# Kernel optimization log

Hardware: AMD Instinct MI355X
Metric: run time of the kernel (lower is better)

## Reference

```python
import jax, jax.numpy as jnp
import numpy as np

B, N, F, H = 1, 778, 128, 8
D = F // H        # per-head dim (d_q = d_v = 16)
D2 = 2 * D        # attn-mlp hidden channels per head (grouped conv: 2*f_dim / H)
EPS = 1e-6


def setup_inputs() -> dict:
    key = jax.random.key(0)
    ks = jax.random.split(key, 16)
    s = 0.02
    def lin(k, i, o):
        return jax.random.normal(k, (i, o), jnp.float32) * s
    f32 = jnp.float32
    return {
        "Lf": jax.random.normal(ks[0], (B, N, F), f32),
        "Rf": jax.random.normal(ks[1], (B, N, F), f32),
        "left_pos": jax.random.normal(ks[2], (B, N, F), f32),
        "right_pos": jax.random.normal(ks[3], (B, N, F), f32),
        # pos_mlp: Linear(F,2F) -> ReLU -> Linear(2F,F)
        "pos_W1": lin(ks[4], F, 2 * F), "pos_b1": jnp.zeros((2 * F,), f32),
        "pos_W2": lin(ks[5], 2 * F, F), "pos_b2": jnp.zeros((F,), f32),
        # q/k/v projections (F -> H*D = F)
        "Wq": lin(ks[6], F, F), "bq": jnp.zeros((F,), f32),
        "Wv": lin(ks[7], F, F), "bv": jnp.zeros((F,), f32),
        "Wk": lin(ks[8], F, F), "bk": jnp.zeros((F,), f32),
        # attn_mlp: grouped 1x1 convs == per-head linear maps D->D2->D
        "conv1_w": jax.random.normal(ks[9], (H, D2, D), f32) * s, "conv1_b": jnp.zeros((H, D2), f32),
        "conv2_w": jax.random.normal(ks[10], (H, D, D2), f32) * s, "conv2_b": jnp.zeros((H, D), f32),
        # ffL = MLP_res_block: LayerNorm + Linear(F,2F)->ReLU->Linear(2F,F) + residual
        "ln_g": jnp.ones((F,), f32), "ln_b": jnp.zeros((F,), f32),
        "ff_W1": lin(ks[11], F, 2 * F), "ff_b1": jnp.zeros((2 * F,), f32),
        "ff_W2": lin(ks[12], 2 * F, F), "ff_b2": jnp.zeros((F,), f32),
    }


def reference(Lf, Rf, left_pos, right_pos,
              pos_W1, pos_b1, pos_W2, pos_b2,
              Wq, bq, Wv, bv, Wk, bk,
              conv1_w, conv1_b, conv2_w, conv2_b,
              ln_g, ln_b, ff_W1, ff_b1, ff_W2, ff_b2):
    b, n, f = Lf.shape
    # pairwise relative positions -> per-pair embedding via pos MLP
    rel_pos = left_pos[:, :, None, :] - right_pos[:, None, :, :]          # (b,i,j,F)
    rel = jax.nn.relu(rel_pos @ pos_W1 + pos_b1) @ pos_W2 + pos_b2        # (b,i,j,F)
    rel = rel.reshape(b, n, n, H, D)                                       # (b,i,j,h,d)
    Lq = (Lf @ Wq + bq).reshape(b, n, H, D)
    Lv = (Lf @ Wv + bv).reshape(b, n, H, D)
    Rk = (Rf @ Wk + bk).reshape(b, n, H, D)
    # subtraction-based pairwise scores + rel-pos embedding
    x = Lq[:, :, None] - Rk[:, None, :] + rel                              # (b,i,j,h,d)
    # grouped 1x1 convs == independent per-head linears over channel d
    hid = jax.nn.relu(jnp.einsum('bijhd,hod->bijho', x, conv1_w) + conv1_b)
    sim = jnp.einsum('bijho,hdo->bijhd', hid, conv2_w) + conv2_b           # (b,i,j,h,d)
    # torch softmax(dim=-2) on (b, h*d, i, j) -> over i
    attn = jax.nn.softmax(sim, axis=1)
    # NOTE: v = repeat(Lv, 'b h j d -> b h i j d') broadcasts Lv over i (indexed by j)
    v = Lv[:, None] + rel                                                  # (b,i,j,h,d)
    agg = jnp.einsum('bijhd,bijhd->bihd', attn, v).reshape(b, n, f)        # sum over j
    y = Lf + agg  # dropout is identity in eval
    # MLP_res_block: x + fc2(relu(fc1(LN(x))))
    mu = jnp.mean(y, axis=-1, keepdims=True)
    var = jnp.var(y, axis=-1, keepdims=True)
    yn = (y - mu) / jnp.sqrt(var + EPS) * ln_g + ln_b
    return y + (jax.nn.relu(yn @ ff_W1 + ff_b1) @ ff_W2 + ff_b2)
```

## Files before the change

### kernel.cpp

```cpp
#include <hip/hip_runtime.h>
#include <hip/hip_bf16.h>

#define NROW 778
#define NPAD 784
#define FDIM 128
#define KHID 256

typedef unsigned short u16;
typedef __attribute__((ext_vector_type(4))) unsigned int u32x4;
typedef __attribute__((ext_vector_type(4))) float f32x4;

__device__ __forceinline__ u16 f2bfu(float x) {
  return __builtin_bit_cast(u16, __float2bfloat16(x));
}

__device__ __forceinline__ void mfma_bf16(f32x4& d, const u32x4& a, const u32x4& b) {
  asm("v_mfma_f32_16x16x32_bf16 %0, %1, %2, %0" : "+v"(d) : "v"(a), "v"(b));
}

#define WS_A    0u
#define WS_C    802816u
#define WS_XI   1605632u
#define WS_XJ   2007040u
#define WS_VJ   2408448u
#define WS_S    2809856u
#define WS_INV  3211264u
#define WS_AGG  3612672u
#define WS_W2B  4014080u
#define WS_C1B  4079616u
#define WS_C2B  4096000u

#define SM_A    0
#define SM_CF   16384
#define SM_W2B  32768
#define SM_HID  0
#define SM_XJ   65536
#define SM_SP   73728
#define SM_INVS 73728
#define SM_VJ   81920
#define SM_C1B  98304
#define SM_C2B  114688
#define SM_X    122880
#define SM_CB1  155648
#define SM_CB2  156672
#define SM_TOTAL 157184

__global__ void kzero(float* S, float* agg) {
  int idx = blockIdx.x * blockDim.x + threadIdx.x;
  if (idx < NPAD * FDIM) { S[idx] = 0.f; agg[idx] = 0.f; }
}

__global__ void kinv(const float* __restrict__ S, float* __restrict__ invS) {
  int idx = blockIdx.x * blockDim.x + threadIdx.x;
  if (idx >= NPAD * FDIM) return;
  int j = idx >> 7;
  invS[idx] = (j < NROW) ? 1.f / S[idx] : 0.f;
}

__global__ void kprep_rows(const float* __restrict__ Lf, const float* __restrict__ Rf,
                           const float* __restrict__ lp, const float* __restrict__ rp,
                           const float* __restrict__ W1, const float* __restrict__ b1,
                           const float* __restrict__ b2,
                           const float* __restrict__ Wq, const float* __restrict__ bq,
                           const float* __restrict__ Wv, const float* __restrict__ bv,
                           const float* __restrict__ Wk, const float* __restrict__ bk,
                           float* __restrict__ a, float* __restrict__ c,
                           float* __restrict__ xi, float* __restrict__ xj,
                           float* __restrict__ vj) {
  __shared__ float sl[128], sr[128], slp[128], srp[128];
  const int row = blockIdx.x, t = threadIdx.x;
  if (t < 128) {
    sl[t] = Lf[row * 128 + t]; sr[t] = Rf[row * 128 + t];
    slp[t] = lp[row * 128 + t]; srp[t] = rp[row * 128 + t];
  }
  __syncthreads();
  float aa = 0.f, cc = 0.f;
  for (int k = 0; k < 128; ++k) {
    float w = W1[k * 256 + t];
    aa += slp[k] * w; cc += srp[k] * w;
  }
  a[row * 256 + t] = aa;
  c[row * 256 + t] = b1[t] - cc;
  if (t < 128) {
    float q = 0.f, kk = 0.f, vv = 0.f;
    for (int k = 0; k < 128; ++k) {
      float l = sl[k], r = sr[k];
      q  += l * Wq[k * 128 + t];
      vv += l * Wv[k * 128 + t];
      kk += r * Wk[k * 128 + t];
    }
    xi[row * 128 + t] = q + bq[t] + b2[t];
    xj[row * 128 + t] = -(kk + bk[t]);
    vj[row * 128 + t] = vv + bv[t] + b2[t];
  }
}

__global__ void kprep_frags(const float* __restrict__ W2, const float* __restrict__ c1w,
                            const float* __restrict__ c2w,
                            u16* __restrict__ w2B, u16* __restrict__ c1B,
                            u16* __restrict__ c2B) {
  const int idx0 = blockIdx.x * blockDim.x + threadIdx.x;
  const int nthr = gridDim.x * blockDim.x;
  for (int idx = idx0; idx < 32768; idx += nthr) {
    int e = idx & 7, ln = (idx >> 3) & 63, n = (idx >> 9) & 7, ks = idx >> 12;
    int k = ks * 32 + ((ln >> 4) << 3) + e;
    int col = n * 16 + (ln & 15);
    w2B[idx] = f2bfu(W2[k * FDIM + col]);
  }
  for (int idx = idx0; idx < 8192; idx += nthr) {
    int e = idx & 7, ln = (idx >> 3) & 63, b = (idx >> 9) & 3, hp = idx >> 11;
    int k = ((ln >> 4) << 3) + e;
    int col = ln & 15;
    int hb = hp * 2 + (b >> 1);
    float v = ((k >> 4) == (b >> 1)) ? c1w[(hb * 32 + (b & 1) * 16 + col) * 16 + (k & 15)] : 0.f;
    c1B[idx] = f2bfu(v);
  }
  for (int idx = idx0; idx < 4096; idx += nthr) {
    int e = idx & 7, ln = (idx >> 3) & 63, h = idx >> 9;
    int o = ((ln >> 4) << 3) + e;
    int d = ln & 15;
    c2B[idx] = f2bfu(c2w[(h * 16 + d) * 32 + o]);
  }
}

template <int PASS>
__global__ __launch_bounds__(512, 2) void kpass(
    const float* __restrict__ ga, const float* __restrict__ gc,
    const float* __restrict__ gxi, const float* __restrict__ gxj,
    const float* __restrict__ gvj, const u16* __restrict__ gw2B,
    const u16* __restrict__ gc1B, const u16* __restrict__ gc2B,
    const float* __restrict__ gcb1, const float* __restrict__ gcb2,
    float* __restrict__ S, const float* __restrict__ invS, float* __restrict__ agg) {
  __shared__ __align__(16) char sm[SM_TOTAL];
  float* sA   = (float*)(sm + SM_A);
  float* sCf  = (float*)(sm + SM_CF);
  u16*   sW2B = (u16*)(sm + SM_W2B);
  u16*   sHid = (u16*)(sm + SM_HID);
  float* sXj  = (float*)(sm + SM_XJ);
  float* sSp  = (float*)(sm + SM_SP);
  float* sInvS= (float*)(sm + SM_INVS);
  float* sVj  = (float*)(sm + SM_VJ);
  u16*   sC1B = (u16*)(sm + SM_C1B);
  u16*   sC2B = (u16*)(sm + SM_C2B);
  u16*   sX   = (u16*)(sm + SM_X);
  float* sCB1 = (float*)(sm + SM_CB1);
  float* sCB2 = (float*)(sm + SM_CB2);

  const int tid = threadIdx.x;
  const int lane = tid & 63;
  const int w = tid >> 6;
  const int jj = lane & 15, kg = lane >> 4;
  const int i0 = blockIdx.x * 16, j0 = blockIdx.y * 16;

  for (int idx = tid; idx < 4096; idx += 512) {
    int row = idx >> 8;
    int ir = i0 + row; if (ir > NROW - 1) ir = NROW - 1;
    sA[idx] = ga[ir * KHID + (idx & 255)];
  }
  for (int idx = tid; idx < 4096; idx += 512) {
    int ks = idx >> 9, ln = (idx >> 3) & 63, e = idx & 7;
    int jr = j0 + (ln & 15); if (jr > NROW - 1) jr = NROW - 1;
    int k = ks * 32 + ((ln >> 4) << 3) + e;
    sCf[idx] = gc[jr * KHID + k];
  }
  {
    const u32x4* g = (const u32x4*)gw2B; u32x4* s = (u32x4*)sW2B;
    for (int idx = tid; idx < 4096; idx += 512) s[idx] = g[idx];
    const u32x4* g1 = (const u32x4*)gc1B; u32x4* s1 = (u32x4*)sC1B;
    for (int idx = tid; idx < 1024; idx += 512) s1[idx] = g1[idx];
    const u32x4* g2 = (const u32x4*)gc2B; u32x4* s2 = (u32x4*)sC2B;
    s2[tid] = g2[tid];
    if (tid < 256) sCB1[tid] = gcb1[tid];
    else if (tid < 384) sCB2[tid - 256] = gcb2[tid - 256];
  }
  __syncthreads();

  f32x4 acc[2][8];
#pragma unroll
  for (int mt = 0; mt < 2; ++mt)
#pragma unroll
    for (int n = 0; n < 8; ++n) acc[mt][n] = f32x4{0.f, 0.f, 0.f, 0.f};

#pragma unroll
  for (int ks = 0; ks < 8; ++ks) {
    const float4 c0 = *(const float4*)&sCf[(ks * 64 + lane) * 8];
    const float4 c1 = *(const float4*)&sCf[(ks * 64 + lane) * 8 + 4];
    const int ko = ks * 32 + kg * 8;
    u32x4 A[2];
#pragma unroll
    for (int mt = 0; mt < 2; ++mt) {
      const float4 a0 = *(const float4*)&sA[(2 * w + mt) * KHID + ko];
      const float4 a1 = *(const float4*)&sA[(2 * w + mt) * KHID + ko + 4];
      float h0 = fmaxf(a0.x + c0.x, 0.f), h1 = fmaxf(a0.y + c0.y, 0.f);
      float h2 = fmaxf(a0.z + c0.z, 0.f), h3 = fmaxf(a0.w + c0.w, 0.f);
      float h4 = fmaxf(a1.x + c1.x, 0.f), h5 = fmaxf(a1.y + c1.y, 0.f);
      float h6 = fmaxf(a1.z + c1.z, 0.f), h7 = fmaxf(a1.w + c1.w, 0.f);
      A[mt] = u32x4{(unsigned)f2bfu(h0) | ((unsigned)f2bfu(h1) << 16),
                    (unsigned)f2bfu(h2) | ((unsigned)f2bfu(h3) << 16),
                    (unsigned)f2bfu(h4) | ((unsigned)f2bfu(h5) << 16),
                    (unsigned)f2bfu(h6) | ((unsigned)f2bfu(h7) << 16)};
    }
#pragma unroll
    for (int n = 0; n < 8; ++n) {
      u32x4 B = ((const u32x4*)sW2B)[(ks * 8 + n) * 64 + lane];
      mfma_bf16(acc[0][n], A[0], B);
      mfma_bf16(acc[1][n], A[1], B);
    }
  }
  __syncthreads();

  if (PASS == 0) {
    for (int idx = tid; idx < 2048; idx += 512) sSp[idx] = 0.f;
  } else {
    for (int idx = tid; idx < 2048; idx += 512) {
      int row = idx >> 7, ch = idx & 127;
      int jr = j0 + row;
      sInvS[idx] = invS[jr * FDIM + ch];
      int jc = jr > NROW - 1 ? NROW - 1 : jr;
      sVj[idx] = gvj[jc * FDIM + ch];
    }
  }
  for (int idx = tid; idx < 2048; idx += 512) {
    int row = idx >> 7, ch = idx & 127;
    int jr = j0 + row; if (jr > NROW - 1) jr = NROW - 1;
    sXj[idx] = gxj[jr * FDIM + ch];
  }
  __syncthreads();

  u16* myX = sX + w * 2048;
  u16* myH = sHid + w * 4096;
#pragma unroll
  for (int mt = 0; mt < 2; ++mt) {
    const int i = i0 + 2 * w + mt;
    const int ic = i > NROW - 1 ? NROW - 1 : i;
#pragma unroll
    for (int n = 0; n < 8; ++n) {
      const int ch = n * 16 + jj;
      const float xiv = gxi[ic * FDIM + ch];
#pragma unroll
      for (int r = 0; r < 4; ++r) {
        const int prow = kg * 4 + r;
        float xv = acc[mt][n][r] + xiv + sXj[prow * FDIM + ch];
        int idxX = ((ch >> 5) * 512) + (prow + 16 * ((ch >> 3) & 3)) * 8 + (ch & 7);
        myX[idxX] = f2bfu(xv);
      }
    }
#pragma unroll
    for (int hp = 0; hp < 4; ++hp) {
      u32x4 Ax = ((const u32x4*)myX)[hp * 64 + lane];
#pragma unroll
      for (int b = 0; b < 4; ++b) {
        u32x4 Bw = ((const u32x4*)sC1B)[(hp * 4 + b) * 64 + lane];
        f32x4 hacc = f32x4{0.f, 0.f, 0.f, 0.f};
        mfma_bf16(hacc, Ax, Bw);
        const int och = (hp * 2 + (b >> 1)) * 32 + (b & 1) * 16 + jj;
        const float bias = sCB1[och];
#pragma unroll
        for (int r = 0; r < 4; ++r) {
          const int prow = kg * 4 + r;
          float hv = fmaxf(hacc[r] + bias, 0.f);
          int idxH = ((och >> 5) * 512) + (prow + 16 * ((och >> 3) & 3)) * 8 + (och & 7);
          myH[idxH] = f2bfu(hv);
        }
      }
    }
#pragma unroll
    for (int h = 0; h < 8; ++h) {
      u32x4 Ah = ((const u32x4*)myH)[h * 64 + lane];
      u32x4 Bw = ((const u32x4*)sC2B)[h * 64 + lane];
      f32x4 sacc = f32x4{0.f, 0.f, 0.f, 0.f};
      mfma_bf16(sacc, Ah, Bw);
      const float bias = sCB2[h * 16 + jj];
      if (PASS == 0) {
        if (i < NROW) {
#pragma unroll
          for (int r = 0; r < 4; ++r) {
            float e = __expf(sacc[r] + bias);
            atomicAdd(&sSp[(kg * 4 + r) * FDIM + h * 16 + jj], e);
          }
        }
      } else {
        float sum = 0.f;
#pragma unroll
        for (int r = 0; r < 4; ++r) {
          const int prow = kg * 4 + r;
          float e = __expf(sacc[r] + bias);
          float iv = sInvS[prow * FDIM + h * 16 + jj];
          float vv = acc[mt][h][r] + sVj[prow * FDIM + h * 16 + jj];
          sum += e * iv * vv;
        }
        sum += __shfl_xor(sum, 16);
        sum += __shfl_xor(sum, 32);
        if (lane < 16) atomicAdd(&agg[i * FDIM + h * 16 + lane], sum);
      }
    }
  }
  if (PASS == 0) {
    __syncthreads();
    for (int idx = tid; idx < 2048; idx += 512) {
      int row = idx >> 7;
      atomicAdd(&S[(j0 + row) * FDIM + (idx & 127)], sSp[idx]);
    }
  }
}

__global__ void kfinal(const float* __restrict__ Lf, const float* __restrict__ agg,
                       const float* __restrict__ g, const float* __restrict__ b,
                       const float* __restrict__ W1, const float* __restrict__ b1,
                       const float* __restrict__ W2, const float* __restrict__ b2,
                       float* __restrict__ out) {
  __shared__ float sY[128], sYn[128], sH[256], sStat[2];
  const int row = blockIdx.x, t = threadIdx.x;
  if (t < 128) sY[t] = Lf[row * 128 + t] + agg[row * 128 + t];
  __syncthreads();
  if (t < 64) {
    float y0 = sY[t], y1 = sY[t + 64];
    float s = y0 + y1, s2 = y0 * y0 + y1 * y1;
#pragma unroll
    for (int off = 32; off; off >>= 1) {
      s += __shfl_down(s, off);
      s2 += __shfl_down(s2, off);
    }
    if (t == 0) {
      float mu = s * (1.f / 128.f);
      float var = s2 * (1.f / 128.f) - mu * mu;
      sStat[0] = mu;
      sStat[1] = rsqrtf(var + 1e-6f);
    }
  }
  __syncthreads();
  if (t < 128) sYn[t] = (sY[t] - sStat[0]) * sStat[1] * g[t] + b[t];
  __syncthreads();
  float ha = b1[t];
  for (int k = 0; k < 128; ++k) ha += sYn[k] * W1[k * 256 + t];
  sH[t] = fmaxf(ha, 0.f);
  __syncthreads();
  if (t < 128) {
    float oa = b2[t];
    for (int k = 0; k < 256; ++k) oa += sH[k] * W2[k * 128 + t];
    out[row * 128 + t] = sY[t] + oa;
  }
}

extern "C" void kernel_launch(void* const* d_in, const int* in_sizes, int n_in,
                              void* d_out, int out_size, void* d_ws, size_t ws_size,
                              hipStream_t stream) {
  const float* Lf  = (const float*)d_in[0];
  const float* Rf  = (const float*)d_in[1];
  const float* lp  = (const float*)d_in[2];
  const float* rp  = (const float*)d_in[3];
  const float* pW1 = (const float*)d_in[4];
  const float* pb1 = (const float*)d_in[5];
  const float* pW2 = (const float*)d_in[6];
  const float* pb2 = (const float*)d_in[7];
  const float* Wq  = (const float*)d_in[8];
  const float* bq  = (const float*)d_in[9];
  const float* Wv  = (const float*)d_in[10];
  const float* bv  = (const float*)d_in[11];
  const float* Wk  = (const float*)d_in[12];
  const float* bk  = (const float*)d_in[13];
  const float* c1w = (const float*)d_in[14];
  const float* c1b = (const float*)d_in[15];
  const float* c2w = (const float*)d_in[16];
  const float* c2b = (const float*)d_in[17];
  const float* lng = (const float*)d_in[18];
  const float* lnb = (const float*)d_in[19];
  const float* fW1 = (const float*)d_in[20];
  const float* fb1 = (const float*)d_in[21];
  const float* fW2 = (const float*)d_in[22];
  const float* fb2 = (const float*)d_in[23];
  float* out = (float*)d_out;
  char* ws = (char*)d_ws;

  float* a    = (float*)(ws + WS_A);
  float* c    = (float*)(ws + WS_C);
  float* xi   = (float*)(ws + WS_XI);
  float* xj   = (float*)(ws + WS_XJ);
  float* vj   = (float*)(ws + WS_VJ);
  float* S    = (float*)(ws + WS_S);
  float* invS = (float*)(ws + WS_INV);
  float* agg  = (float*)(ws + WS_AGG);
  u16* w2B = (u16*)(ws + WS_W2B);
  u16* c1B = (u16*)(ws + WS_C1B);
  u16* c2B = (u16*)(ws + WS_C2B);

  kzero<<<dim3((NPAD * FDIM + 511) / 512), dim3(512), 0, stream>>>(S, agg);
  kprep_rows<<<dim3(NROW), dim3(256), 0, stream>>>(Lf, Rf, lp, rp, pW1, pb1, pb2,
                                                   Wq, bq, Wv, bv, Wk, bk,
                                                   a, c, xi, xj, vj);
  kprep_frags<<<dim3(16), dim3(512), 0, stream>>>(pW2, c1w, c2w, w2B, c1B, c2B);

  kpass<0><<<dim3(49, 49), dim3(512), 0, stream>>>(a, c, xi, xj, vj, w2B, c1B, c2B,
                                                   c1b, c2b, S, invS, agg);
  kinv<<<dim3((NPAD * FDIM + 511) / 512), dim3(512), 0, stream>>>(S, invS);
  kpass<1><<<dim3(49, 49), dim3(512), 0, stream>>>(a, c, xi, xj, vj, w2B, c1B, c2B,
                                                   c1b, c2b, S, invS, agg);
  kfinal<<<dim3(NROW), dim3(256), 0, stream>>>(Lf, agg, lng, lnb, fW1, fb1, fW2, fb2, out);
}
```

Measured before the change: 756.1 us.

## Make pass kernels persistent over tile strips with register accumulation

Shrinks each pass grid from 49x49 to 49x5 blocks. Each block keeps one tile fixed (j in pass 0, i in pass 1) and loops over a strided set of the other-axis tiles, so the fixed operand is loaded once per block. Softmax denominators and aggregation partials now accumulate in registers across iterations, which removes most shared and global atomics. Weight fragments and biases are read straight from global memory instead of being staged in LDS, trading global/L2 traffic for less staging work. The cost is only 245 blocks per pass, which risks underfilling the GPU and adds serial work per block.

```diff
diff --git a/kernel.cpp b/kernel.cpp
--- a/kernel.cpp
+++ b/kernel.cpp
@@ -13,8 +13,7 @@
 __device__ __forceinline__ u16 f2bfu(float x) {
   return __builtin_bit_cast(u16, __float2bfloat16(x));
 }
-
-__device__ __forceinline__ void mfma_bf16(f32x4& d, const u32x4& a, const u32x4& b) {
+__device__ __forceinline__ void mfma32(f32x4& d, const u32x4& a, const u32x4& b) {
   asm("v_mfma_f32_16x16x32_bf16 %0, %1, %2, %0" : "+v"(d) : "v"(a), "v"(b));
 }
 
@@ -29,21 +28,6 @@
 #define WS_W2B  4014080u
 #define WS_C1B  4079616u
 #define WS_C2B  4096000u
-
-#define SM_A    0
-#define SM_CF   16384
-#define SM_W2B  32768
-#define SM_HID  0
-#define SM_XJ   65536
-#define SM_SP   73728
-#define SM_INVS 73728
-#define SM_VJ   81920
-#define SM_C1B  98304
-#define SM_C2B  114688
-#define SM_X    122880
-#define SM_CB1  155648
-#define SM_CB2  156672
-#define SM_TOTAL 157184
 
 __global__ void kzero(float* S, float* agg) {
   int idx = blockIdx.x * blockDim.x + threadIdx.x;
@@ -131,175 +115,217 @@
     const u16* __restrict__ gc1B, const u16* __restrict__ gc2B,
     const float* __restrict__ gcb1, const float* __restrict__ gcb2,
     float* __restrict__ S, const float* __restrict__ invS, float* __restrict__ agg) {
-  __shared__ __align__(16) char sm[SM_TOTAL];
-  float* sA   = (float*)(sm + SM_A);
-  float* sCf  = (float*)(sm + SM_CF);
-  u16*   sW2B = (u16*)(sm + SM_W2B);
-  u16*   sHid = (u16*)(sm + SM_HID);
-  float* sXj  = (float*)(sm + SM_XJ);
-  float* sSp  = (float*)(sm + SM_SP);
-  float* sInvS= (float*)(sm + SM_INVS);
-  float* sVj  = (float*)(sm + SM_VJ);
-  u16*   sC1B = (u16*)(sm + SM_C1B);
-  u16*   sC2B = (u16*)(sm + SM_C2B);
-  u16*   sX   = (u16*)(sm + SM_X);
-  float* sCB1 = (float*)(sm + SM_CB1);
-  float* sCB2 = (float*)(sm + SM_CB2);
+  __shared__ __align__(16) char sm[155648];
+  float* sA  = (float*)(sm + 0);
+  float* sCf = (float*)(sm + 16384);
+  float* sXj = (float*)(sm + 131072);
+  float* sIv = (float*)(sm + 139264);
+  float* sVj = (float*)(sm + 147456);
 
   const int tid = threadIdx.x;
   const int lane = tid & 63;
   const int w = tid >> 6;
   const int jj = lane & 15, kg = lane >> 4;
-  const int i0 = blockIdx.x * 16, j0 = blockIdx.y * 16;
-
-  for (int idx = tid; idx < 4096; idx += 512) {
-    int row = idx >> 8;
-    int ir = i0 + row; if (ir > NROW - 1) ir = NROW - 1;
-    sA[idx] = ga[ir * KHID + (idx & 255)];
-  }
-  for (int idx = tid; idx < 4096; idx += 512) {
-    int ks = idx >> 9, ln = (idx >> 3) & 63, e = idx & 7;
-    int jr = j0 + (ln & 15); if (jr > NROW - 1) jr = NROW - 1;
-    int k = ks * 32 + ((ln >> 4) << 3) + e;
-    sCf[idx] = gc[jr * KHID + k];
-  }
-  {
-    const u32x4* g = (const u32x4*)gw2B; u32x4* s = (u32x4*)sW2B;
-    for (int idx = tid; idx < 4096; idx += 512) s[idx] = g[idx];
-    const u32x4* g1 = (const u32x4*)gc1B; u32x4* s1 = (u32x4*)sC1B;
-    for (int idx = tid; idx < 1024; idx += 512) s1[idx] = g1[idx];
-    const u32x4* g2 = (const u32x4*)gc2B; u32x4* s2 = (u32x4*)sC2B;
-    s2[tid] = g2[tid];
-    if (tid < 256) sCB1[tid] = gcb1[tid];
-    else if (tid < 384) sCB2[tid - 256] = gcb2[tid - 256];
-  }
-  __syncthreads();
-
-  f32x4 acc[2][8];
-#pragma unroll
-  for (int mt = 0; mt < 2; ++mt)
-#pragma unroll
-    for (int n = 0; n < 8; ++n) acc[mt][n] = f32x4{0.f, 0.f, 0.f, 0.f};
-
-#pragma unroll
-  for (int ks = 0; ks < 8; ++ks) {
-    const float4 c0 = *(const float4*)&sCf[(ks * 64 + lane) * 8];
-    const float4 c1 = *(const float4*)&sCf[(ks * 64 + lane) * 8 + 4];
-    const int ko = ks * 32 + kg * 8;
-    u32x4 A[2];
-#pragma unroll
-    for (int mt = 0; mt < 2; ++mt) {
-      const float4 a0 = *(const float4*)&sA[(2 * w + mt) * KHID + ko];
-      const float4 a1 = *(const float4*)&sA[(2 * w + mt) * KHID + ko + 4];
-      float h0 = fmaxf(a0.x + c0.x, 0.f), h1 = fmaxf(a0.y + c0.y, 0.f);
-      float h2 = fmaxf(a0.z + c0.z, 0.f), h3 = fmaxf(a0.w + c0.w, 0.f);
-      float h4 = fmaxf(a1.x + c1.x, 0.f), h5 = fmaxf(a1.y + c1.y, 0.f);
-      float h6 = fmaxf(a1.z + c1.z, 0.f), h7 = fmaxf(a1.w + c1.w, 0.f);
-      A[mt] = u32x4{(unsigned)f2bfu(h0) | ((unsigned)f2bfu(h1) << 16),
-                    (unsigned)f2bfu(h2) | ((unsigned)f2bfu(h3) << 16),
-                    (unsigned)f2bfu(h4) | ((unsigned)f2bfu(h5) << 16),
-                    (unsigned)f2bfu(h6) | ((unsigned)f2bfu(h7) << 16)};
-    }
-#pragma unroll
-    for (int n = 0; n < 8; ++n) {
-      u32x4 B = ((const u32x4*)sW2B)[(ks * 8 + n) * 64 + lane];
-      mfma_bf16(acc[0][n], A[0], B);
-      mfma_bf16(acc[1][n], A[1], B);
-    }
-  }
-  __syncthreads();
+  const int fix0 = blockIdx.x * 16;
+  const int s = blockIdx.y;
+
+  u16* myX = (u16*)(sm + 32768 + w * 12288);
+  u16* myH = (u16*)(sm + 32768 + w * 12288 + 4096);
+  const u32x4* w2v = (const u32x4*)gw2B;
+  const u32x4* c1v = (const u32x4*)gc1B;
+  const u32x4* c2v = (const u32x4*)gc2B;
 
   if (PASS == 0) {
-    for (int idx = tid; idx < 2048; idx += 512) sSp[idx] = 0.f;
-  } else {
+    const int j0 = fix0;
+    for (int idx = tid; idx < 4096; idx += 512) {
+      int ks = idx >> 9, ln = (idx >> 3) & 63, e = idx & 7;
+      int jr = j0 + (ln & 15); if (jr > NROW - 1) jr = NROW - 1;
+      int k = ks * 32 + ((ln >> 4) << 3) + e;
+      sCf[idx] = gc[jr * KHID + k];
+    }
     for (int idx = tid; idx < 2048; idx += 512) {
       int row = idx >> 7, ch = idx & 127;
-      int jr = j0 + row;
-      sInvS[idx] = invS[jr * FDIM + ch];
-      int jc = jr > NROW - 1 ? NROW - 1 : jr;
-      sVj[idx] = gvj[jc * FDIM + ch];
-    }
-  }
-  for (int idx = tid; idx < 2048; idx += 512) {
-    int row = idx >> 7, ch = idx & 127;
-    int jr = j0 + row; if (jr > NROW - 1) jr = NROW - 1;
-    sXj[idx] = gxj[jr * FDIM + ch];
-  }
-  __syncthreads();
-
-  u16* myX = sX + w * 2048;
-  u16* myH = sHid + w * 4096;
-#pragma unroll
-  for (int mt = 0; mt < 2; ++mt) {
-    const int i = i0 + 2 * w + mt;
-    const int ic = i > NROW - 1 ? NROW - 1 : i;
-#pragma unroll
-    for (int n = 0; n < 8; ++n) {
-      const int ch = n * 16 + jj;
-      const float xiv = gxi[ic * FDIM + ch];
-#pragma unroll
-      for (int r = 0; r < 4; ++r) {
-        const int prow = kg * 4 + r;
-        float xv = acc[mt][n][r] + xiv + sXj[prow * FDIM + ch];
-        int idxX = ((ch >> 5) * 512) + (prow + 16 * ((ch >> 3) & 3)) * 8 + (ch & 7);
-        myX[idxX] = f2bfu(xv);
-      }
-    }
-#pragma unroll
-    for (int hp = 0; hp < 4; ++hp) {
-      u32x4 Ax = ((const u32x4*)myX)[hp * 64 + lane];
-#pragma unroll
-      for (int b = 0; b < 4; ++b) {
-        u32x4 Bw = ((const u32x4*)sC1B)[(hp * 4 + b) * 64 + lane];
-        f32x4 hacc = f32x4{0.f, 0.f, 0.f, 0.f};
-        mfma_bf16(hacc, Ax, Bw);
-        const int och = (hp * 2 + (b >> 1)) * 32 + (b & 1) * 16 + jj;
-        const float bias = sCB1[och];
+      int jr = j0 + row; if (jr > NROW - 1) jr = NROW - 1;
+      sXj[idx] = gxj[jr * FDIM + ch];
+    }
+  } else {
+    const int i0 = fix0;
+    for (int idx = tid; idx < 4096; idx += 512) {
+      int row = idx >> 8;
+      int ir = i0 + row; if (ir > NROW - 1) ir = NROW - 1;
+      sA[idx] = ga[ir * KHID + (idx & 255)];
+    }
+  }
+
+  float ssum[8][4];
+  f32x4 asum[2][2];
+  float aacc[2][8];
+#pragma unroll
+  for (int h = 0; h < 8; ++h)
+#pragma unroll
+    for (int r = 0; r < 4; ++r) ssum[h][r] = 0.f;
+#pragma unroll
+  for (int mt = 0; mt < 2; ++mt)
+#pragma unroll
+    for (int h = 0; h < 8; ++h) aacc[mt][h] = 0.f;
+  (void)asum;
+
+  for (int t = s; t < 49; t += 5) {
+    const int i0 = (PASS == 0) ? t * 16 : fix0;
+    const int j0 = (PASS == 0) ? fix0 : t * 16;
+    if (PASS == 0) {
+      for (int idx = tid; idx < 4096; idx += 512) {
+        int row = idx >> 8;
+        int ir = i0 + row; if (ir > NROW - 1) ir = NROW - 1;
+        sA[idx] = ga[ir * KHID + (idx & 255)];
+      }
+    } else {
+      for (int idx = tid; idx < 4096; idx += 512) {
+        int ks = idx >> 9, ln = (idx >> 3) & 63, e = idx & 7;
+        int jr = j0 + (ln & 15); if (jr > NROW - 1) jr = NROW - 1;
+        int k = ks * 32 + ((ln >> 4) << 3) + e;
+        sCf[idx] = gc[jr * KHID + k];
+      }
+      for (int idx = tid; idx < 2048; idx += 512) {
+        int row = idx >> 7, ch = idx & 127;
+        int jr = j0 + row; if (jr > NROW - 1) jr = NROW - 1;
+        sXj[idx] = gxj[jr * FDIM + ch];
+      }
+      for (int idx = tid; idx < 2048; idx += 512) {
+        int row = idx >> 7, ch = idx & 127;
+        int jr = j0 + row;
+        sIv[idx] = invS[jr * FDIM + ch];
+        int jc = jr > NROW - 1 ? NROW - 1 : jr;
+        sVj[idx] = gvj[jc * FDIM + ch];
+      }
+    }
+    __syncthreads();
+
+    f32x4 acc[2][8];
+#pragma unroll
+    for (int mt = 0; mt < 2; ++mt)
+#pragma unroll
+      for (int n = 0; n < 8; ++n) acc[mt][n] = f32x4{0.f, 0.f, 0.f, 0.f};
+
+#pragma unroll
+    for (int ks = 0; ks < 8; ++ks) {
+      const float4 c0 = *(const float4*)&sCf[(ks * 64 + lane) * 8];
+      const float4 c1 = *(const float4*)&sCf[(ks * 64 + lane) * 8 + 4];
+      const int ko = ks * 32 + kg * 8;
+      u32x4 A[2];
+#pragma unroll
+      for (int mt = 0; mt < 2; ++mt) {
+        const float4 a0 = *(const float4*)&sA[(2 * w + mt) * KHID + ko];
+        const float4 a1 = *(const float4*)&sA[(2 * w + mt) * KHID + ko + 4];
+        float h0 = fmaxf(a0.x + c0.x, 0.f), h1 = fmaxf(a0.y + c0.y, 0.f);
+        float h2 = fmaxf(a0.z + c0.z, 0.f), h3 = fmaxf(a0.w + c0.w, 0.f);
+        float h4 = fmaxf(a1.x + c1.x, 0.f), h5 = fmaxf(a1.y + c1.y, 0.f);
+        float h6 = fmaxf(a1.z + c1.z, 0.f), h7 = fmaxf(a1.w + c1.w, 0.f);
+        A[mt] = u32x4{(unsigned)f2bfu(h0) | ((unsigned)f2bfu(h1) << 16),
+                      (unsigned)f2bfu(h2) | ((unsigned)f2bfu(h3) << 16),
+                      (unsigned)f2bfu(h4) | ((unsigned)f2bfu(h5) << 16),
+                      (unsigned)f2bfu(h6) | ((unsigned)f2bfu(h7) << 16)};
+      }
+#pragma unroll
+      for (int n = 0; n < 8; ++n) {
+        u32x4 B = w2v[(ks * 8 + n) * 64 + lane];
+        mfma32(acc[0][n], A[0], B);
+        mfma32(acc[1][n], A[1], B);
+      }
+    }
+
+#pragma unroll
+    for (int mt = 0; mt < 2; ++mt) {
+      const int i = i0 + 2 * w + mt;
+      const int ic = i > NROW - 1 ? NROW - 1 : i;
+#pragma unroll
+      for (int n = 0; n < 8; ++n) {
+        const int ch = n * 16 + jj;
+        const float xiv = gxi[ic * FDIM + ch];
 #pragma unroll
         for (int r = 0; r < 4; ++r) {
           const int prow = kg * 4 + r;
-          float hv = fmaxf(hacc[r] + bias, 0.f);
-          int idxH = ((och >> 5) * 512) + (prow + 16 * ((och >> 3) & 3)) * 8 + (och & 7);
-          myH[idxH] = f2bfu(hv);
+          float xv = acc[mt][n][r] + xiv + sXj[prow * FDIM + ch];
+          int idxX = ((ch >> 5) * 512) + (prow + 16 * ((ch >> 3) & 3)) * 8 + (ch & 7);
+          myX[idxX] = f2bfu(xv);
         }
       }
-    }
-#pragma unroll
-    for (int h = 0; h < 8; ++h) {
-      u32x4 Ah = ((const u32x4*)myH)[h * 64 + lane];
-      u32x4 Bw = ((const u32x4*)sC2B)[h * 64 + lane];
-      f32x4 sacc = f32x4{0.f, 0.f, 0.f, 0.f};
-      mfma_bf16(sacc, Ah, Bw);
-      const float bias = sCB2[h * 16 + jj];
-      if (PASS == 0) {
-        if (i < NROW) {
+#pragma unroll
+      for (int hp = 0; hp < 4; ++hp) {
+        u32x4 Ax = ((const u32x4*)myX)[hp * 64 + lane];
+#pragma unroll
+        for (int b = 0; b < 4; ++b) {
+          u32x4 Bw = c1v[(hp * 4 + b) * 64 + lane];
+          f32x4 hacc = f32x4{0.f, 0.f, 0.f, 0.f};
+          mfma32(hacc, Ax, Bw);
+          const int och = (hp * 2 + (b >> 1)) * 32 + (b & 1) * 16 + jj;
+          const float bias = gcb1[och];
 #pragma unroll
           for (int r = 0; r < 4; ++r) {
-            float e = __expf(sacc[r] + bias);
-            atomicAdd(&sSp[(kg * 4 + r) * FDIM + h * 16 + jj], e);
+            const int prow = kg * 4 + r;
+            float hv = fmaxf(hacc[r] + bias, 0.f);
+            int idxH = ((och >> 5) * 512) + (prow + 16 * ((och >> 3) & 3)) * 8 + (och & 7);
+            myH[idxH] = f2bfu(hv);
           }
         }
-      } else {
-        float sum = 0.f;
-#pragma unroll
-        for (int r = 0; r < 4; ++r) {
-          const int prow = kg * 4 + r;
-          float e = __expf(sacc[r] + bias);
-          float iv = sInvS[prow * FDIM + h * 16 + jj];
-          float vv = acc[mt][h][r] + sVj[prow * FDIM + h * 16 + jj];
-          sum += e * iv * vv;
+      }
+#pragma unroll
+      for (int h = 0; h < 8; ++h) {
+        u32x4 Ah = ((const u32x4*)myH)[h * 64 + lane];
+        u32x4 Bw = c2v[h * 64 + lane];
+        f32x4 sacc = f32x4{0.f, 0.f, 0.f, 0.f};
+        mfma32(sacc, Ah, Bw);
+        const float bias = gcb2[h * 16 + jj];
+        if (PASS == 0) {
+          if (i < NROW) {
+#pragma unroll
+            for (int r = 0; r < 4; ++r) {
+              ssum[h][r] += __expf(sacc[r] + bias);
+            }
+          }
+        } else {
+          float sum = 0.f;
+#pragma unroll
+          for (int r = 0; r < 4; ++r) {
+            const int prow = kg * 4 + r;
+            float e = __expf(sacc[r] + bias);
+            float iv = sIv[prow * FDIM + h * 16 + jj];
+            float vv = acc[mt][h][r] + sVj[prow * FDIM + h * 16 + jj];
+            sum += e * iv * vv;
+          }
+          sum += __shfl_xor(sum, 16);
+          sum += __shfl_xor(sum, 32);
+          aacc[mt][h] += sum;
         }
-        sum += __shfl_xor(sum, 16);
-        sum += __shfl_xor(sum, 32);
-        if (lane < 16) atomicAdd(&agg[i * FDIM + h * 16 + lane], sum);
-      }
-    }
-  }
+      }
+    }
+    __syncthreads();
+  }
+
   if (PASS == 0) {
+    float* strips = (float*)sm;
+#pragma unroll
+    for (int h = 0; h < 8; ++h)
+#pragma unroll
+      for (int r = 0; r < 4; ++r)
+        strips[w * 2048 + (kg * 4 + r) * FDIM + h * 16 + jj] = ssum[h][r];
     __syncthreads();
+    const int j0 = fix0;
     for (int idx = tid; idx < 2048; idx += 512) {
-      int row = idx >> 7;
-      atomicAdd(&S[(j0 + row) * FDIM + (idx & 127)], sSp[idx]);
+      float v = 0.f;
+#pragma unroll
+      for (int ww = 0; ww < 8; ++ww) v += strips[ww * 2048 + idx];
+      atomicAdd(&S[(j0 + (idx >> 7)) * FDIM + (idx & 127)], v);
+    }
+  } else {
+    const int i0 = fix0;
+#pragma unroll
+    for (int mt = 0; mt < 2; ++mt) {
+      const int i = i0 + 2 * w + mt;
+#pragma unroll
+      for (int h = 0; h < 8; ++h) {
+        if (lane < 16) atomicAdd(&agg[i * FDIM + h * 16 + lane], aacc[mt][h]);
+      }
     }
   }
 }
@@ -390,10 +416,10 @@
                                                    a, c, xi, xj, vj);
   kprep_frags<<<dim3(16), dim3(512), 0, stream>>>(pW2, c1w, c2w, w2B, c1B, c2B);
 
-  kpass<0><<<dim3(49, 49), dim3(512), 0, stream>>>(a, c, xi, xj, vj, w2B, c1B, c2B,
-                                                   c1b, c2b, S, invS, agg);
+  kpass<0><<<dim3(49, 5), dim3(512), 0, stream>>>(a, c, xi, xj, vj, w2B, c1B, c2B,
+                                                  c1b, c2b, S, invS, agg);
   kinv<<<dim3((NPAD * FDIM + 511) / 512), dim3(512), 0, stream>>>(S, invS);
-  kpass<1><<<dim3(49, 49), dim3(512), 0, stream>>>(a, c, xi, xj, vj, w2B, c1B, c2B,
-                                                   c1b, c2b, S, invS, agg);
+  kpass<1><<<dim3(49, 5), dim3(512), 0, stream>>>(a, c, xi, xj, vj, w2B, c1B, c2B,
+                                                  c1b, c2b, S, invS, agg);
   kfinal<<<dim3(NROW), dim3(256), 0, stream>>>(Lf, agg, lng, lnb, fW1, fb1, fW2, fb2, out);
 }
```

Measured after the change: 0.9996 ms. 32.2% more time.
